# Performance work log

Hardware: AMD Instinct MI355X
Metric: run time of the kernel (lower is better)

## Reference

```python
import jax, jax.numpy as jnp
import numpy as np

EPS = 1e-5
NUM_GRAPHS = 64


def _linear(x, W, b):
    return x @ W + b


def setup_inputs() -> dict:
    key = jax.random.key(0)
    ks = jax.random.split(key, 32)
    N, E, IN, EF, H, ED, T, L, C = 25000, 400000, 128, 16, 32, 32, 4, 2, 1
    F = H            # F_in (divide_input=False)
    Fo = H // T      # F_out per tower

    def w(k, shape):
        return jax.random.normal(k, shape, jnp.float32) / np.sqrt(shape[-2])

    inp = {
        'x': jax.random.normal(ks[0], (N, IN), jnp.float32),
        'edge_attr': jax.random.normal(ks[1], (E, EF), jnp.float32),
        'edge_weight': jax.random.uniform(ks[2], (E,), jnp.float32),
        'edge_index': jax.random.randint(ks[3], (2, E), 0, N),
        'batch': jnp.sort(jax.random.randint(ks[4], (N,), 0, NUM_GRAPHS)),
        'node_W': w(ks[5], (IN, H)), 'node_b': jnp.zeros((H,), jnp.float32),
        'edge_W': w(ks[6], (EF, ED)), 'edge_b': jnp.zeros((ED,), jnp.float32),
        'enc_W': w(ks[7], (L, ED, F)), 'enc_b': jnp.zeros((L, F), jnp.float32),
        'pre_W': w(ks[8], (L, T, 3 * F, F)), 'pre_b': jnp.zeros((L, T, F), jnp.float32),
        'post_W': w(ks[9], (L, T, 13 * F, Fo)), 'post_b': jnp.zeros((L, T, Fo), jnp.float32),
        'lin_W': w(ks[10], (L, H, H)), 'lin_b': jnp.zeros((L, H), jnp.float32),
        'bn_g': jnp.ones((L, H), jnp.float32), 'bn_b': jnp.zeros((L, H), jnp.float32),
        'mlp_W1': w(ks[11], (H, H)), 'mlp_b1': jnp.zeros((H,), jnp.float32),
        'mlp_W2': w(ks[12], (H, H // 2)), 'mlp_b2': jnp.zeros((H // 2,), jnp.float32),
        'mlp_W3': w(ks[13], (H // 2, C)), 'mlp_b3': jnp.zeros((C,), jnp.float32),
    }
    return inp


def reference(x, edge_attr, edge_weight, node_W, node_b, edge_W, edge_b,
              enc_W, enc_b, pre_W, pre_b, post_W, post_b, lin_W, lin_b,
              bn_g, bn_b, mlp_W1, mlp_b1, mlp_W2, mlp_b2, mlp_W3, mlp_b3,
              edge_index, batch):
    N = x.shape[0]
    L, T = pre_W.shape[0], pre_W.shape[1]
    src, dst = edge_index[0], edge_index[1]

    # degree-based scalers (PNA): avg_deg_log = mean_n log(deg_n + 1)
    deg = jax.ops.segment_sum(jnp.ones((src.shape[0],), x.dtype), dst, num_segments=N)
    avg_deg_log = jnp.mean(jnp.log(deg + 1.0))
    degc = jnp.clip(deg, 1.0)[:, None, None]          # [N,1,1]
    log_deg = jnp.log(degc + 1.0)
    amp = log_deg / avg_deg_log                        # amplification scaler
    att = avg_deg_log / log_deg                        # attenuation scaler
    has_edge = (deg > 0)[:, None, None]

    h = _linear(x, node_W, node_b)                     # node_emb  [N,H]
    e = _linear(edge_attr, edge_W, edge_b)             # edge_emb  [E,ED]

    for l in range(L):
        el = _linear(e, enc_W[l], enc_b[l])            # edge_encoder [E,F]
        m_in = jnp.concatenate([h[dst], h[src], el], axis=-1)      # [E,3F]
        msg = jnp.einsum('ef,tfg->etg', m_in, pre_W[l]) + pre_b[l]  # per-tower pre_nn [E,T,F]
        msg = msg * edge_weight[:, None, None]
        s = jax.ops.segment_sum(msg, dst, num_segments=N)
        s2 = jax.ops.segment_sum(msg * msg, dst, num_segments=N)
        mean = s / degc
        std = jnp.sqrt(jax.nn.relu(s2 / degc - mean * mean) + EPS)
        mn = jnp.where(has_edge, jax.ops.segment_min(msg, dst, num_segments=N), 0.0)
        mx = jnp.where(has_edge, jax.ops.segment_max(msg, dst, num_segments=N), 0.0)
        agg = jnp.concatenate([mean, mn, mx, std], axis=-1)            # [N,T,4F]
        agg = jnp.concatenate([agg, agg * amp, agg * att], axis=-1)    # [N,T,12F]
        out = jnp.concatenate(
            [jnp.broadcast_to(h[:, None, :], (N, T, h.shape[-1])), agg], axis=-1)  # [N,T,13F]
        out = jnp.einsum('ntf,tfg->ntg', out, post_W[l]) + post_b[l]   # post_nn [N,T,Fo]
        out = out.reshape(N, -1) @ lin_W[l] + lin_b[l]                 # [N,H]
        mu = jnp.mean(out, axis=0)
        var = jnp.var(out, axis=0)
        out = (out - mu) / jnp.sqrt(var + EPS) * bn_g[l] + bn_b[l]     # BatchNorm (batch stats)
        h = jax.nn.relu(out)

    g = jax.ops.segment_sum(h, batch, num_segments=NUM_GRAPHS)        # global_add_pool
    g = jax.nn.relu(_linear(g, mlp_W1, mlp_b1))
    g = jax.nn.relu(_linear(g, mlp_W2, mlp_b2))
    return _linear(g, mlp_W3, mlp_b3)
```

## Files before the change

kernel.cpp:

```cpp
#include <hip/hip_runtime.h>

constexpr float kEps = 1e-5f;

typedef _Float16 h2 __attribute__((ext_vector_type(2)));
typedef float f2v __attribute__((ext_vector_type(2)));

__device__ __forceinline__ unsigned short f2bf(float x) {
  unsigned int u = __float_as_uint(x);
  unsigned int r = (u + 0x7fffu + ((u >> 16) & 1u)) >> 16;
  return (unsigned short)r;
}
__device__ __forceinline__ float bflo(unsigned int u) { return __uint_as_float(u << 16); }
__device__ __forceinline__ float bfhi(unsigned int u) { return __uint_as_float(u & 0xffff0000u); }
__device__ __forceinline__ unsigned int packbf(float a, float b) {
  return (unsigned int)f2bf(a) | ((unsigned int)f2bf(b) << 16);
}
__device__ __forceinline__ unsigned int pkh2(float a, float b) {
  h2 v; v.x = (_Float16)a; v.y = (_Float16)b;
  return __builtin_bit_cast(unsigned int, v);
}
__device__ __forceinline__ float dot2a(h2 a, h2 b, float c) {
#if __has_builtin(__builtin_amdgcn_fdot2)
  return __builtin_amdgcn_fdot2(a, b, c, false);
#else
  return c + (float)a.x * (float)b.x + (float)a.y * (float)b.y;
#endif
}
__device__ __forceinline__ h2 ash2(unsigned int u) { return __builtin_bit_cast(h2, u); }
__device__ __forceinline__ f2v fma2(f2v a, f2v b, f2v c) { return __builtin_elementwise_fma(a, b, c); }
__device__ __forceinline__ f2v unbf2(unsigned int u) { f2v r; r.x = bflo(u); r.y = bfhi(u); return r; }


__global__ void zero_kernel(int* __restrict__ a, int* __restrict__ b,
                            float* __restrict__ bnb, int n) {
  int i = blockIdx.x * blockDim.x + threadIdx.x;
  if (i < n) { a[i] = 0; b[i] = 0; }
  if (i < 128) bnb[i] = 0.f;
}

__global__ void hist_kernel(const int* __restrict__ dst, int* __restrict__ deg, int E) {
  int e = blockIdx.x * blockDim.x + threadIdx.x;
  if (e < E) atomicAdd(&deg[dst[e]], 1);
}

__global__ void scan1_kernel(const int* __restrict__ deg, int* __restrict__ off,
                             int* __restrict__ part, int N) {
  __shared__ int sm[1024];
  int i = blockIdx.x * 1024 + threadIdx.x;
  int v = (i < N) ? deg[i] : 0;
  sm[threadIdx.x] = v;
  __syncthreads();
  for (int o = 1; o < 1024; o <<= 1) {
    int t = (threadIdx.x >= o) ? sm[threadIdx.x - o] : 0;
    __syncthreads();
    sm[threadIdx.x] += t;
    __syncthreads();
  }
  if (i < N) off[i] = sm[threadIdx.x] - v;
  if (threadIdx.x == 1023) part[blockIdx.x] = sm[1023];
}

__global__ void scan2_kernel(int* __restrict__ part, int* __restrict__ off, int nb, int N) {
  if (threadIdx.x == 0) {
    int run = 0;
    for (int b = 0; b < nb; b++) { int p = part[b]; part[b] = run; run += p; }
    off[N] = run;
  }
}

__global__ void scan3_kernel(int* __restrict__ off, const int* __restrict__ part, int N) {
  int i = blockIdx.x * 1024 + threadIdx.x;
  if (i < N) off[i] += part[blockIdx.x];
}

__global__ void fill_kernel(const int* __restrict__ src, const int* __restrict__ dst,
                            const float* __restrict__ ew, const float4* __restrict__ eattr4,
                            const int* __restrict__ off, int* __restrict__ cnt,
                            int* __restrict__ srcs, float* __restrict__ ews,
                            uint4* __restrict__ eg16, int E) {
  int e = blockIdx.x * blockDim.x + threadIdx.x;
  if (e < E) {
    int d = dst[e];
    int slot = off[d] + atomicAdd(&cnt[d], 1);
    srcs[slot] = src[e];
    ews[slot] = ew[e];
    float4 a = eattr4[e * 4 + 0], b = eattr4[e * 4 + 1];
    float4 c = eattr4[e * 4 + 2], q = eattr4[e * 4 + 3];
    uint4 u0, u1;
    u0.x = pkh2(a.x, a.y); u0.y = pkh2(a.z, a.w);
    u0.z = pkh2(b.x, b.y); u0.w = pkh2(b.z, b.w);
    u1.x = pkh2(c.x, c.y); u1.y = pkh2(c.z, c.w);
    u1.z = pkh2(q.x, q.y); u1.w = pkh2(q.z, q.w);
    eg16[(size_t)slot * 2 + 0] = u0;
    eg16[(size_t)slot * 2 + 1] = u1;
  }
}

__global__ void adl_kernel(const int* __restrict__ deg, float* __restrict__ adl, int N) {
  __shared__ float sm[1024];
  float s = 0.f;
  for (int n = threadIdx.x; n < N; n += 1024) s += logf((float)deg[n] + 1.f);
  sm[threadIdx.x] = s;
  __syncthreads();
  for (int o = 512; o > 0; o >>= 1) {
    if (threadIdx.x < o) sm[threadIdx.x] += sm[threadIdx.x + o];
    __syncthreads();
  }
  if (threadIdx.x == 0) adl[0] = sm[0];
}

__global__ void node_emb_kernel(const float* __restrict__ x, const float* __restrict__ W,
                                const float* __restrict__ b, float* __restrict__ h, int N) {
  int n = blockIdx.x * 8 + (threadIdx.x >> 5);
  int j = threadIdx.x & 31;
  if (n >= N) return;
  float acc = b[j];
  const float4* x4 = (const float4*)(x + (size_t)n * 128);
#pragma unroll
  for (int q = 0; q < 32; q++) {
    float4 v = x4[q];
    acc += v.x * W[(4 * q + 0) * 32 + j];
    acc += v.y * W[(4 * q + 1) * 32 + j];
    acc += v.z * W[(4 * q + 2) * 32 + j];
    acc += v.w * W[(4 * q + 3) * 32 + j];
  }
  h[n * 32 + j] = acc;
}

__global__ void fuse_kernel(const float* __restrict__ edge_W, const float* __restrict__ edge_b,
                            const float* __restrict__ enc_W, const float* __restrict__ enc_b,
                            const float* __restrict__ pre_W, const float* __restrict__ pre_b,
                            float* __restrict__ Wf, float* __restrict__ bf) {
  __shared__ float tW[2][16][32];
  __shared__ float tb[2][32];
  int tid = threadIdx.x;
  for (int i = tid; i < 1024; i += 256) {
    int l = i >> 9, r = (i >> 5) & 15, c = i & 31;
    float s = 0.f;
    for (int k = 0; k < 32; k++) s += edge_W[r * 32 + k] * enc_W[(l * 32 + k) * 32 + c];
    tW[l][r][c] = s;
  }
  for (int i = tid; i < 64; i += 256) {
    int l = i >> 5, c = i & 31;
    float s = enc_b[l * 32 + c];
    for (int k = 0; k < 32; k++) s += edge_b[k] * enc_W[(l * 32 + k) * 32 + c];
    tb[l][c] = s;
  }
  __syncthreads();
  for (int i = tid; i < 4096; i += 256) {
    int l = i >> 11, t = (i >> 9) & 3, r = (i >> 5) & 15, c = i & 31;
    float s = 0.f;
    for (int k = 0; k < 32; k++) s += tW[l][r][k] * pre_W[((l * 4 + t) * 96 + 64 + k) * 32 + c];
    Wf[i] = s;
  }
  for (int i = tid; i < 256; i += 256) {
    int l = i >> 7, t = (i >> 5) & 3, c = i & 31;
    float s = pre_b[(l * 4 + t) * 32 + c];
    for (int k = 0; k < 32; k++) s += tb[l][k] * pre_W[((l * 4 + t) * 96 + 64 + k) * 32 + c];
    bf[i] = s;
  }
}

__global__ __launch_bounds__(256) void prep_kernel(
    const float* __restrict__ h, const float* __restrict__ preW,
    const float* __restrict__ bfv, unsigned short* __restrict__ qB,
    unsigned short* __restrict__ AB, int N) {
  __shared__ float hs[16][32];
  int tid = threadIdx.x;
  int c = tid & 127, half = tid >> 7;
  int t = c >> 5, g = c & 31;
  float ws[32], wd[32];
  {
    const float* pS = preW + (t * 96 + 32) * 32 + g;
    const float* pD = preW + (t * 96) * 32 + g;
#pragma unroll
    for (int k = 0; k < 32; k++) { ws[k] = pS[k * 32]; wd[k] = pD[k * 32]; }
  }
  float bc = bfv[c];
  int base = blockIdx.x * 16;
  for (int i = tid; i < 512; i += 256) {
    int nn = i >> 5;
    hs[nn][i & 31] = (base + nn < N) ? h[(size_t)(base + nn) * 32 + (i & 31)] : 0.f;
  }
  __syncthreads();
#pragma unroll
  for (int nn = 0; nn < 8; ++nn) {
    int nl = half + 2 * nn;
    int n = base + nl;
    if (n >= N) continue;
    float qa = 0.f, Aa = bc;
#pragma unroll
    for (int k = 0; k < 32; k++) {
      float hk = hs[nl][k];
      qa = fmaf(hk, ws[k], qa);
      Aa = fmaf(hk, wd[k], Aa);
    }
    qB[(size_t)n * 128 + c] = f2bf(qa);
    AB[(size_t)n * 128 + c] = f2bf(Aa);
  }
}

__global__ __launch_bounds__(256) void bnprep_kernel(
    const float* __restrict__ pre, const float* __restrict__ bnv,
    const float* __restrict__ gamma, const float* __restrict__ beta,
    const float* __restrict__ preW, const float* __restrict__ bfv,
    float* __restrict__ h, unsigned short* __restrict__ qB,
    unsigned short* __restrict__ AB, int N) {
  __shared__ float hs[16][32];
  int tid = threadIdx.x;
  int base = blockIdx.x * 16;
  float invN = 1.f / (float)N;
  for (int idx = tid; idx < 512; idx += 256) {
    int nn = idx >> 5, j = idx & 31;
    int n = base + nn;
    float v = 0.f;
    if (n < N) {
      float mu = bnv[j] * invN;
      float var = bnv[32 + j] * invN - mu * mu;
      float is = rsqrtf(var + kEps);
      v = fmaxf((pre[(size_t)n * 32 + j] - mu) * is * gamma[j] + beta[j], 0.f);
      h[(size_t)n * 32 + j] = v;
    }
    hs[nn][j] = v;
  }
  int c = tid & 127, half = tid >> 7;
  int t = c >> 5, g = c & 31;
  float ws[32], wd[32];
  {
    const float* pS = preW + (t * 96 + 32) * 32 + g;
    const float* pD = preW + (t * 96) * 32 + g;
#pragma unroll
    for (int k = 0; k < 32; k++) { ws[k] = pS[k * 32]; wd[k] = pD[k * 32]; }
  }
  float bc = bfv[c];
  __syncthreads();
#pragma unroll
  for (int nn = 0; nn < 8; ++nn) {
    int nl = half + 2 * nn;
    int n = base + nl;
    if (n >= N) continue;
    float qa = 0.f, Aa = bc;
#pragma unroll
    for (int k = 0; k < 32; k++) {
      float hk = hs[nl][k];
      qa = fmaf(hk, ws[k], qa);
      Aa = fmaf(hk, wd[k], Aa);
    }
    qB[(size_t)n * 128 + c] = f2bf(qa);
    AB[(size_t)n * 128 + c] = f2bf(Aa);
  }
}

#define DOTE(F0, F1, UA, UB)                                         \
  F0 = dot2a(ash2(UA.x), w0[0], F0); F1 = dot2a(ash2(UA.x), w1[0], F1); \
  F0 = dot2a(ash2(UA.y), w0[1], F0); F1 = dot2a(ash2(UA.y), w1[1], F1); \
  F0 = dot2a(ash2(UA.z), w0[2], F0); F1 = dot2a(ash2(UA.z), w1[2], F1); \
  F0 = dot2a(ash2(UA.w), w0[3], F0); F1 = dot2a(ash2(UA.w), w1[3], F1); \
  F0 = dot2a(ash2(UB.x), w0[4], F0); F1 = dot2a(ash2(UB.x), w1[4], F1); \
  F0 = dot2a(ash2(UB.y), w0[5], F0); F1 = dot2a(ash2(UB.y), w1[5], F1); \
  F0 = dot2a(ash2(UB.z), w0[6], F0); F1 = dot2a(ash2(UB.z), w1[6], F1); \
  F0 = dot2a(ash2(UB.w), w0[7], F0); F1 = dot2a(ash2(UB.w), w1[7], F1);

#define STATACC(V0, V1)                                                    \
  s0a += V0; sq0 = fmaf(V0, V0, sq0); mn0 = fminf(mn0, V0); mx0 = fmaxf(mx0, V0); \
  s1a += V1; sq1 = fmaf(V1, V1, sq1); mn1 = fminf(mn1, V1); mx1 = fmaxf(mx1, V1);

__global__ __launch_bounds__(256, 4) void agg10b_kernel(
    const unsigned int* __restrict__ qB, const unsigned int* __restrict__ AB,
    const int* __restrict__ coff, const int* __restrict__ srcs,
    const float* __restrict__ ews, const uint4* __restrict__ eg16,
    const float* __restrict__ Wf, unsigned int* __restrict__ stats, int N) {
  int lane = threadIdx.x & 63;
  int wv = (blockIdx.x * blockDim.x + threadIdx.x) >> 6;
  int nwaves = (gridDim.x * blockDim.x) >> 6;
  int t = lane >> 4, g0 = (2 * lane) & 31;
  h2 w0[8], w1[8];
  {
    const float* p = Wf + t * 512 + g0;
#pragma unroll
    for (int k = 0; k < 8; k++) {
      w0[k].x = (_Float16)p[(2 * k) * 32];     w0[k].y = (_Float16)p[(2 * k + 1) * 32];
      w1[k].x = (_Float16)p[(2 * k) * 32 + 1]; w1[k].y = (_Float16)p[(2 * k + 1) * 32 + 1];
    }
  }
  for (int n = wv; n < N; n += nwaves) {
    unsigned int au = AB[(size_t)n * 64 + lane];
    float a0 = bflo(au), a1 = bfhi(au);
    int beg = coff[n], end = coff[n + 1];
    int dg = end - beg;
    float s0a = 0.f, s1a = 0.f, sq0 = 0.f, sq1 = 0.f;
    float mn0 = 1e30f, mn1 = 1e30f, mx0 = -1e30f, mx1 = -1e30f;

    int i = beg;
    unsigned int q0 = 0, q1 = 0, q2 = 0, q3 = 0;
    int sc0 = 0, sc1 = 0, sc2 = 0, sc3 = 0;
    if (i + 4 <= end) {
      int t0 = srcs[i], t1 = srcs[i + 1], t2 = srcs[i + 2], t3 = srcs[i + 3];
      q0 = qB[(size_t)t0 * 64 + lane];
      q1 = qB[(size_t)t1 * 64 + lane];
      q2 = qB[(size_t)t2 * 64 + lane];
      q3 = qB[(size_t)t3 * 64 + lane];
    }
    if (i + 8 <= end) { sc0 = srcs[i + 4]; sc1 = srcs[i + 5]; sc2 = srcs[i + 6]; sc3 = srcs[i + 7]; }
    for (; i + 4 <= end; i += 4) {
      unsigned int nq0 = 0, nq1 = 0, nq2 = 0, nq3 = 0;
      if (i + 8 <= end) {
        nq0 = qB[(size_t)sc0 * 64 + lane];
        nq1 = qB[(size_t)sc1 * 64 + lane];
        nq2 = qB[(size_t)sc2 * 64 + lane];
        nq3 = qB[(size_t)sc3 * 64 + lane];
      }
      float w0s = ews[i], w1s = ews[i + 1], w2s = ews[i + 2], w3s = ews[i + 3];
      const uint4* ep = eg16 + (size_t)i * 2;
      uint4 eA0 = ep[0], eA1 = ep[1], eB0 = ep[2], eB1 = ep[3];
      uint4 eC0 = ep[4], eC1 = ep[5], eD0 = ep[6], eD1 = ep[7];
      if (i + 12 <= end) { sc0 = srcs[i + 8]; sc1 = srcs[i + 9]; sc2 = srcs[i + 10]; sc3 = srcs[i + 11]; }
      float f00 = 0.f, f10 = 0.f, f01 = 0.f, f11 = 0.f;
      float f02 = 0.f, f12 = 0.f, f03 = 0.f, f13 = 0.f;
      DOTE(f00, f10, eA0, eA1)
      DOTE(f01, f11, eB0, eB1)
      DOTE(f02, f12, eC0, eC1)
      DOTE(f03, f13, eD0, eD1)
      float v0, v1;
      v0 = (a0 + bflo(q0) + f00) * w0s; v1 = (a1 + bfhi(q0) + f10) * w0s; STATACC(v0, v1)
      v0 = (a0 + bflo(q1) + f01) * w1s; v1 = (a1 + bfhi(q1) + f11) * w1s; STATACC(v0, v1)
      v0 = (a0 + bflo(q2) + f02) * w2s; v1 = (a1 + bfhi(q2) + f12) * w2s; STATACC(v0, v1)
      v0 = (a0 + bflo(q3) + f03) * w3s; v1 = (a1 + bfhi(q3) + f13) * w3s; STATACC(v0, v1)
      q0 = nq0; q1 = nq1; q2 = nq2; q3 = nq3;
    }
    for (; i < end; ++i) {
      int s = srcs[i];
      unsigned int q = qB[(size_t)s * 64 + lane];
      float w = ews[i];
      const uint4* ep = eg16 + (size_t)i * 2;
      uint4 ea = ep[0], eb = ep[1];
      float f0 = 0.f, f1 = 0.f;
      DOTE(f0, f1, ea, eb)
      float v0 = (a0 + bflo(q) + f0) * w;
      float v1 = (a1 + bfhi(q) + f1) * w;
      STATACC(v0, v1)
    }
    if (dg == 0) { mn0 = 0.f; mx0 = 0.f; mn1 = 0.f; mx1 = 0.f; }
    float inv = 1.f / (float)(dg > 0 ? dg : 1);
    float mean0 = s0a * inv, mean1 = s1a * inv;
    float sd0 = sqrtf(fmaxf(sq0 * inv - mean0 * mean0, 0.f) + kEps);
    float sd1 = sqrtf(fmaxf(sq1 * inv - mean1 * mean1, 0.f) + kEps);
    unsigned int* sp = stats + (size_t)n * 256;
    sp[0 * 64 + lane] = packbf(mean0, mean1);
    sp[1 * 64 + lane] = packbf(mn0, mn1);
    sp[2 * 64 + lane] = packbf(mx0, mx1);
    sp[3 * 64 + lane] = packbf(sd0, sd1);
  }
}

__global__ __launch_bounds__(256) void post_kernel(
    const float* __restrict__ h, const unsigned int* __restrict__ stats,
    const int* __restrict__ coff, const float* __restrict__ adl,
    const float* __restrict__ postW, const float* __restrict__ postB,
    const float* __restrict__ linW, const float* __restrict__ linB,
    float* __restrict__ pre, float* __restrict__ bn, int N) {
  __shared__ unsigned int pwp[208 * 32];
  __shared__ unsigned int stu[4][256];
  __shared__ float red[8][32];
  int tid = threadIdx.x;
  for (int i = tid; i < 6656; i += 256) {
    int r = i >> 5, cc = i & 31, tP = cc >> 3, gq = cc & 7;
    float lo = postW[tP * 3328 + (2 * r) * 8 + gq];
    float hi = postW[tP * 3328 + (2 * r + 1) * 8 + gq];
    pwp[i] = packbf(lo, hi);
  }
  __syncthreads();

  int wave = tid >> 6, lane = tid & 63;
  int c = lane & 31, hh = lane >> 5;
  int tP = c >> 3;
  float adN = adl[0];
  float bs = 0.f, bq = 0.f;

  for (int n = blockIdx.x * 4 + wave; n < N; n += gridDim.x * 4) {
    {
      uint4 su = ((const uint4*)stats)[(size_t)n * 64 + lane];
      ((uint4*)stu[wave])[lane] = su;
    }
    int dg = coff[n + 1] - coff[n];
    float degc = (float)(dg > 0 ? dg : 1);
    float ad = adN / (float)N;
    float ld = logf(degc + 1.f);
    float amp = ld / ad, att = ad / ld;

    float acc = (hh == 0) ? postB[tP * 8 + (c & 7)] : 0.f;
    const float4* h4 = (const float4*)(h + (size_t)n * 32);
#pragma unroll
    for (int q4 = 0; q4 < 4; q4++) {
      float4 hv = h4[hh * 4 + q4];
      int r0 = hh * 8 + q4 * 2;
      unsigned int u0 = pwp[r0 * 32 + c], u1 = pwp[(r0 + 1) * 32 + c];
      acc = fmaf(hv.x, bflo(u0), acc);
      acc = fmaf(hv.y, bfhi(u0), acc);
      acc = fmaf(hv.z, bflo(u1), acc);
      acc = fmaf(hv.w, bfhi(u1), acc);
    }
    f2v ym, ya, yt;
    ym.x = 0.f; ym.y = 0.f; ya = ym; yt = ym;
#pragma unroll 8
    for (int jj = 0; jj < 32; jj++) {
      int sIdx = hh * 2 + (jj >> 4);
      unsigned int sv = stu[wave][sIdx * 64 + tP * 16 + (jj & 15)];
      f2v v2 = unbf2(sv);
      int rm = 16 + hh * 32 + jj;
      f2v um = unbf2(pwp[rm * 32 + c]);
      f2v ua = unbf2(pwp[(rm + 64) * 32 + c]);
      f2v ut = unbf2(pwp[(rm + 128) * 32 + c]);
      ym = fma2(v2, um, ym);
      ya = fma2(v2, ua, ya);
      yt = fma2(v2, ut, yt);
    }
    acc += ym.x + ym.y;
    acc = fmaf(amp, ya.x + ya.y, acc);
    acc = fmaf(att, yt.x + yt.y, acc);
    acc += __shfl_xor(acc, 32);
    float o = linB[c];
#pragma unroll
    for (int k = 0; k < 32; k++) {
      float a = __shfl(acc, k);
      o = fmaf(a, linW[k * 32 + c], o);
    }
    if (lane < 32) {
      pre[(size_t)n * 32 + c] = o;
      bs += o;
      bq = fmaf(o, o, bq);
    }
  }

  __syncthreads();
  if (lane < 32) {
    red[wave * 2 + 0][c] = bs;
    red[wave * 2 + 1][c] = bq;
  }
  __syncthreads();
  if (tid < 64) {
    int which = tid >> 5, cc = tid & 31;
    float s = red[0 * 2 + which][cc] + red[1 * 2 + which][cc] +
              red[2 * 2 + which][cc] + red[3 * 2 + which][cc];
    atomicAdd(&bn[which * 32 + cc], s);
  }
}


__device__ __forceinline__ int lower_bound_dev(const int* a, int n, int key) {
  int lo = 0, hi = n;
  while (lo < hi) {
    int m = (lo + hi) >> 1;
    if (a[m] < key) lo = m + 1; else hi = m;
  }
  return lo;
}

__global__ void pool2_kernel(const float* __restrict__ pre, const float* __restrict__ bnv,
                             const float* __restrict__ gamma, const float* __restrict__ beta,
                             const int* __restrict__ batch, float* __restrict__ gp, int N) {
  int gi = blockIdx.x;
  int lo = lower_bound_dev(batch, N, gi);
  int hi = lower_bound_dev(batch, N, gi + 1);
  __shared__ float part[8][32];
  int j = threadIdx.x & 31, ch = threadIdx.x >> 5;
  float invN = 1.f / (float)N;
  float mu = bnv[j] * invN;
  float var = bnv[32 + j] * invN - mu * mu;
  float is = rsqrtf(var + kEps);
  float gm = gamma[j], bt = beta[j];
  float s = 0.f;
  for (int n = lo + ch; n < hi; n += 8)
    s += fmaxf((pre[(size_t)n * 32 + j] - mu) * is * gm + bt, 0.f);
  part[ch][j] = s;
  __syncthreads();
  if (threadIdx.x < 32) {
    float t = 0.f;
    for (int c2 = 0; c2 < 8; c2++) t += part[c2][j];
    gp[gi * 32 + j] = t;
  }
}

__global__ void mlp_kernel(const float* __restrict__ gp,
                           const float* __restrict__ W1, const float* __restrict__ b1,
                           const float* __restrict__ W2, const float* __restrict__ b2,
                           const float* __restrict__ W3, const float* __restrict__ b3,
                           float* __restrict__ out) {
  __shared__ float g1[64 * 32];
  __shared__ float g2[64 * 16];
  int tid = threadIdx.x;
  for (int i = tid; i < 2048; i += 256) {
    int r = i >> 5, c = i & 31;
    float s = b1[c];
    for (int k = 0; k < 32; k++) s += gp[r * 32 + k] * W1[k * 32 + c];
    g1[i] = fmaxf(s, 0.f);
  }
  __syncthreads();
  for (int i = tid; i < 1024; i += 256) {
    int r = i >> 4, c = i & 15;
    float s = b2[c];
    for (int k = 0; k < 32; k++) s += g1[r * 32 + k] * W2[k * 16 + c];
    g2[i] = fmaxf(s, 0.f);
  }
  __syncthreads();
  if (tid < 64) {
    float s = b3[0];
    for (int k = 0; k < 16; k++) s += g2[tid * 16 + k] * W3[k];
    out[tid] = s;
  }
}


extern "C" void kernel_launch(void* const* d_in, const int* in_sizes, int n_in,
                              void* d_out, int out_size, void* d_ws, size_t ws_size,
                              hipStream_t stream) {
  (void)n_in; (void)out_size; (void)ws_size;
  const float* x     = (const float*)d_in[0];
  const float* eattr = (const float*)d_in[1];
  const float* ew    = (const float*)d_in[2];
  const int*   eidx  = (const int*)d_in[3];
  const int*   batch = (const int*)d_in[4];
  const float* nodeW = (const float*)d_in[5];
  const float* nodeB = (const float*)d_in[6];
  const float* edgeW = (const float*)d_in[7];
  const float* edgeB = (const float*)d_in[8];
  const float* encW  = (const float*)d_in[9];
  const float* encB  = (const float*)d_in[10];
  const float* preW  = (const float*)d_in[11];
  const float* preB  = (const float*)d_in[12];
  const float* postW = (const float*)d_in[13];
  const float* postB = (const float*)d_in[14];
  const float* linW  = (const float*)d_in[15];
  const float* linB  = (const float*)d_in[16];
  const float* bnG   = (const float*)d_in[17];
  const float* bnB   = (const float*)d_in[18];
  const float* W1    = (const float*)d_in[19];
  const float* b1    = (const float*)d_in[20];
  const float* W2    = (const float*)d_in[21];
  const float* b2    = (const float*)d_in[22];
  const float* W3    = (const float*)d_in[23];
  const float* b3    = (const float*)d_in[24];
  float* out = (float*)d_out;

  int N = in_sizes[0] / 128;
  int E = in_sizes[2];
  const int* srcp = eidx;
  const int* dstp = eidx + E;

  char* wsb = (char*)d_ws;
  size_t woff = 0;
  auto alloc = [&](size_t bytes) -> void* {
    void* p = (void*)(wsb + woff);
    woff += (bytes + 255) & ~(size_t)255;
    return p;
  };
  int* deg   = (int*)alloc((size_t)N * 4);
  int* cnt   = (int*)alloc((size_t)N * 4);
  int* coff  = (int*)alloc((size_t)(N + 1) * 4);
  int* part  = (int*)alloc(64 * 4);
  int* srcs  = (int*)alloc((size_t)E * 4);
  float* ews = (float*)alloc((size_t)E * 4);
  unsigned int* eg16 = (unsigned int*)alloc((size_t)E * 32);
  float* h    = (float*)alloc((size_t)N * 32 * 4);
  float* pre  = (float*)alloc((size_t)N * 32 * 4);
  float* adl  = (float*)alloc(256);
  float* bnbuf = (float*)alloc(2 * 64 * 4);
  float* gp   = (float*)alloc(64 * 32 * 4);
  float* WfB  = (float*)alloc(2 * 4 * 16 * 32 * 4);
  float* bfB  = (float*)alloc(2 * 4 * 32 * 4);
  unsigned short* qB  = (unsigned short*)alloc((size_t)N * 128 * 2);
  unsigned short* AB  = (unsigned short*)alloc((size_t)N * 128 * 2);
  unsigned int* stats = (unsigned int*)alloc((size_t)N * 256 * 4);

  int nb = (N + 1023) / 1024;
  zero_kernel<<<(N + 255) / 256, 256, 0, stream>>>(deg, cnt, bnbuf, N);
  hist_kernel<<<(E + 255) / 256, 256, 0, stream>>>(dstp, deg, E);
  scan1_kernel<<<nb, 1024, 0, stream>>>(deg, coff, part, N);
  scan2_kernel<<<1, 64, 0, stream>>>(part, coff, nb, N);
  scan3_kernel<<<nb, 1024, 0, stream>>>(coff, part, N);
  fill_kernel<<<(E + 255) / 256, 256, 0, stream>>>(srcp, dstp, ew, (const float4*)eattr,
                                                   coff, cnt, srcs, ews, (uint4*)eg16, E);
  adl_kernel<<<1, 1024, 0, stream>>>(deg, adl, N);
  node_emb_kernel<<<(N + 7) / 8, 256, 0, stream>>>(x, nodeW, nodeB, h, N);
  fuse_kernel<<<1, 256, 0, stream>>>(edgeW, edgeB, encW, encB, preW, preB, WfB, bfB);

  prep_kernel<<<(N + 15) / 16, 256, 0, stream>>>(h, preW, bfB, qB, AB, N);
  agg10b_kernel<<<2048, 256, 0, stream>>>(
      (const unsigned int*)qB, (const unsigned int*)AB, coff, srcs, ews,
      (const uint4*)eg16, WfB, stats, N);
  post_kernel<<<640, 256, 0, stream>>>(
      h, stats, coff, adl, postW, postB, linW, linB, pre, bnbuf, N);
  bnprep_kernel<<<(N + 15) / 16, 256, 0, stream>>>(
      pre, bnbuf, bnG, bnB, preW + 12288, bfB + 128, h, qB, AB, N);
  agg10b_kernel<<<2048, 256, 0, stream>>>(
      (const unsigned int*)qB, (const unsigned int*)AB, coff, srcs, ews,
      (const uint4*)eg16, WfB + 2048, stats, N);
  post_kernel<<<640, 256, 0, stream>>>(
      h, stats, coff, adl, postW + 13312, postB + 32, linW + 1024, linB + 32,
      pre, bnbuf + 64, N);
  pool2_kernel<<<64, 256, 0, stream>>>(pre, bnbuf + 64, bnG + 32, bnB + 32, batch, gp, N);
  mlp_kernel<<<1, 256, 0, stream>>>(gp, W1, b1, W2, b2, W3, b3, out);
}
```

Baseline: 375.4 us.

## Fold post_nn into lin weights and compute post stage with bf16 MFMA

Precomputes a combined post_W×lin_W matrix per layer, split into identity, amplification and attenuation sections and laid out as bf16 MFMA B-fragments, plus a fused bias. The per-node post stage becomes a 16-node-tile GEMM using 16x16x32 bf16 MFMA over the aggregated statistics and a new bf16 copy of h, with the degree scalers applied after accumulation. This replaces the scalar per-node FMA loop and the shuffle-based lin matvec. The cost is an extra bf16 h buffer written in the prep kernels, a small weight-fusion kernel, and bf16 rounding of the fused weights.

```diff
diff --git a/kernel.cpp b/kernel.cpp
--- a/kernel.cpp
+++ b/kernel.cpp
@@ -4,6 +4,8 @@
 
 typedef _Float16 h2 __attribute__((ext_vector_type(2)));
 typedef float f2v __attribute__((ext_vector_type(2)));
+typedef short bf16x8 __attribute__((ext_vector_type(8)));
+typedef float f32x4v __attribute__((ext_vector_type(4)));
 
 __device__ __forceinline__ unsigned short f2bf(float x) {
   unsigned int u = __float_as_uint(x);
@@ -27,8 +29,10 @@
 #endif
 }
 __device__ __forceinline__ h2 ash2(unsigned int u) { return __builtin_bit_cast(h2, u); }
-__device__ __forceinline__ f2v fma2(f2v a, f2v b, f2v c) { return __builtin_elementwise_fma(a, b, c); }
-__device__ __forceinline__ f2v unbf2(unsigned int u) { f2v r; r.x = bflo(u); r.y = bfhi(u); return r; }
+__device__ __forceinline__ f32x4v mfma16(uint4 a, uint4 b, f32x4v c) {
+  return __builtin_amdgcn_mfma_f32_16x16x32_bf16(
+      __builtin_bit_cast(bf16x8, a), __builtin_bit_cast(bf16x8, b), c, 0, 0, 0);
+}
 
 
 __global__ void zero_kernel(int* __restrict__ a, int* __restrict__ b,
@@ -161,10 +165,51 @@
   }
 }
 
+__global__ void fuse2_kernel(const float* __restrict__ postW_, const float* __restrict__ postB_,
+                             const float* __restrict__ linW_, const float* __restrict__ linB_,
+                             unsigned int* __restrict__ Bfrag, float* __restrict__ bias2) {
+  int l = blockIdx.x;
+  const float* postW = postW_ + (size_t)l * 13312;
+  const float* postB = postB_ + l * 32;
+  const float* linW = linW_ + l * 1024;
+  const float* linB = linB_ + l * 32;
+  unsigned int* Bf = Bfrag + (size_t)l * 26112;
+  int tid = threadIdx.x;
+  for (int idx = tid; idx < 26112; idx += 256) {
+    int d = idx & 3, lane = (idx >> 2) & 63;
+    int ks = (idx >> 8) % 17, jt = (idx >> 8) / 17;
+    int jcol = (jt & 1) * 16 + (lane & 15);
+    int jsec = jt >> 1;
+    float v[2];
+#pragma unroll
+    for (int e2 = 0; e2 < 2; ++e2) {
+      int k = ks * 32 + ((lane >> 4) << 3) + 2 * d + e2;
+      float s = 0.f;
+      if (k < 512) {
+        int st = k >> 7, t = (k >> 5) & 3, g = k & 31;
+        int rowW = 32 + jsec * 128 + st * 32 + g;
+        for (int q = 0; q < 8; ++q)
+          s += postW[t * 3328 + rowW * 8 + q] * linW[(t * 8 + q) * 32 + jcol];
+      } else if (jsec == 0) {
+        int kk = k - 512;
+        for (int c = 0; c < 32; ++c)
+          s += postW[(c >> 3) * 3328 + kk * 8 + (c & 7)] * linW[c * 32 + jcol];
+      }
+      v[e2] = s;
+    }
+    Bf[idx] = packbf(v[0], v[1]);
+  }
+  if (tid < 32) {
+    float s = linB[tid];
+    for (int c = 0; c < 32; ++c) s += postB[c] * linW[c * 32 + tid];
+    bias2[l * 32 + tid] = s;
+  }
+}
+
 __global__ __launch_bounds__(256) void prep_kernel(
     const float* __restrict__ h, const float* __restrict__ preW,
     const float* __restrict__ bfv, unsigned short* __restrict__ qB,
-    unsigned short* __restrict__ AB, int N) {
+    unsigned short* __restrict__ AB, unsigned int* __restrict__ hB, int N) {
   __shared__ float hs[16][32];
   int tid = threadIdx.x;
   int c = tid & 127, half = tid >> 7;
@@ -183,6 +228,11 @@
     hs[nn][i & 31] = (base + nn < N) ? h[(size_t)(base + nn) * 32 + (i & 31)] : 0.f;
   }
   __syncthreads();
+  {
+    int nn = tid >> 4, w = tid & 15;
+    int n = base + nn;
+    if (n < N) hB[(size_t)n * 16 + w] = packbf(hs[nn][2 * w], hs[nn][2 * w + 1]);
+  }
 #pragma unroll
   for (int nn = 0; nn < 8; ++nn) {
     int nl = half + 2 * nn;
@@ -205,7 +255,7 @@
     const float* __restrict__ gamma, const float* __restrict__ beta,
     const float* __restrict__ preW, const float* __restrict__ bfv,
     float* __restrict__ h, unsigned short* __restrict__ qB,
-    unsigned short* __restrict__ AB, int N) {
+    unsigned short* __restrict__ AB, unsigned int* __restrict__ hB, int N) {
   __shared__ float hs[16][32];
   int tid = threadIdx.x;
   int base = blockIdx.x * 16;
@@ -234,6 +284,11 @@
   }
   float bc = bfv[c];
   __syncthreads();
+  {
+    int nn = tid >> 4, w = tid & 15;
+    int n = base + nn;
+    if (n < N) hB[(size_t)n * 16 + w] = packbf(hs[nn][2 * w], hs[nn][2 * w + 1]);
+  }
 #pragma unroll
   for (int nn = 0; nn < 8; ++nn) {
     int nl = half + 2 * nn;
@@ -353,96 +408,75 @@
   }
 }
 
-__global__ __launch_bounds__(256) void post_kernel(
-    const float* __restrict__ h, const unsigned int* __restrict__ stats,
+__global__ __launch_bounds__(256) void postm_kernel(
+    const uint4* __restrict__ statsU4, const uint4* __restrict__ hBU4,
     const int* __restrict__ coff, const float* __restrict__ adl,
-    const float* __restrict__ postW, const float* __restrict__ postB,
-    const float* __restrict__ linW, const float* __restrict__ linB,
-    float* __restrict__ pre, float* __restrict__ bn, int N) {
-  __shared__ unsigned int pwp[208 * 32];
-  __shared__ unsigned int stu[4][256];
-  __shared__ float red[8][32];
-  int tid = threadIdx.x;
-  for (int i = tid; i < 6656; i += 256) {
-    int r = i >> 5, cc = i & 31, tP = cc >> 3, gq = cc & 7;
-    float lo = postW[tP * 3328 + (2 * r) * 8 + gq];
-    float hi = postW[tP * 3328 + (2 * r + 1) * 8 + gq];
-    pwp[i] = packbf(lo, hi);
-  }
-  __syncthreads();
-
-  int wave = tid >> 6, lane = tid & 63;
-  int c = lane & 31, hh = lane >> 5;
-  int tP = c >> 3;
-  float adN = adl[0];
-  float bs = 0.f, bq = 0.f;
-
-  for (int n = blockIdx.x * 4 + wave; n < N; n += gridDim.x * 4) {
-    {
-      uint4 su = ((const uint4*)stats)[(size_t)n * 64 + lane];
-      ((uint4*)stu[wave])[lane] = su;
-    }
-    int dg = coff[n + 1] - coff[n];
-    float degc = (float)(dg > 0 ? dg : 1);
-    float ad = adN / (float)N;
-    float ld = logf(degc + 1.f);
-    float amp = ld / ad, att = ad / ld;
-
-    float acc = (hh == 0) ? postB[tP * 8 + (c & 7)] : 0.f;
-    const float4* h4 = (const float4*)(h + (size_t)n * 32);
-#pragma unroll
-    for (int q4 = 0; q4 < 4; q4++) {
-      float4 hv = h4[hh * 4 + q4];
-      int r0 = hh * 8 + q4 * 2;
-      unsigned int u0 = pwp[r0 * 32 + c], u1 = pwp[(r0 + 1) * 32 + c];
-      acc = fmaf(hv.x, bflo(u0), acc);
-      acc = fmaf(hv.y, bfhi(u0), acc);
-      acc = fmaf(hv.z, bflo(u1), acc);
-      acc = fmaf(hv.w, bfhi(u1), acc);
-    }
-    f2v ym, ya, yt;
-    ym.x = 0.f; ym.y = 0.f; ya = ym; yt = ym;
-#pragma unroll 8
-    for (int jj = 0; jj < 32; jj++) {
-      int sIdx = hh * 2 + (jj >> 4);
-      unsigned int sv = stu[wave][sIdx * 64 + tP * 16 + (jj & 15)];
-      f2v v2 = unbf2(sv);
-      int rm = 16 + hh * 32 + jj;
-      f2v um = unbf2(pwp[rm * 32 + c]);
-      f2v ua = unbf2(pwp[(rm + 64) * 32 + c]);
-      f2v ut = unbf2(pwp[(rm + 128) * 32 + c]);
-      ym = fma2(v2, um, ym);
-      ya = fma2(v2, ua, ya);
-      yt = fma2(v2, ut, yt);
-    }
-    acc += ym.x + ym.y;
-    acc = fmaf(amp, ya.x + ya.y, acc);
-    acc = fmaf(att, yt.x + yt.y, acc);
-    acc += __shfl_xor(acc, 32);
-    float o = linB[c];
-#pragma unroll
-    for (int k = 0; k < 32; k++) {
-      float a = __shfl(acc, k);
-      o = fmaf(a, linW[k * 32 + c], o);
-    }
-    if (lane < 32) {
-      pre[(size_t)n * 32 + c] = o;
-      bs += o;
-      bq = fmaf(o, o, bq);
-    }
-  }
-
-  __syncthreads();
-  if (lane < 32) {
-    red[wave * 2 + 0][c] = bs;
-    red[wave * 2 + 1][c] = bq;
-  }
-  __syncthreads();
-  if (tid < 64) {
-    int which = tid >> 5, cc = tid & 31;
-    float s = red[0 * 2 + which][cc] + red[1 * 2 + which][cc] +
-              red[2 * 2 + which][cc] + red[3 * 2 + which][cc];
-    atomicAdd(&bn[which * 32 + cc], s);
+    const unsigned int* __restrict__ BfragL, const float* __restrict__ bias2,
+    float* __restrict__ pre, float* __restrict__ bn, int N, int ntcnt) {
+  __shared__ uint4 Bs[6 * 6 * 64];
+  int tid = threadIdx.x, wave = tid >> 6, lane = tid & 63;
+  int nt = blockIdx.x * 4 + wave;
+  int ntb = nt * 16;
+  int ntbC = (nt < ntcnt ? nt : ntcnt - 1) * 16;
+  const uint4* Bf4 = (const uint4*)BfragL;
+
+  f32x4v acc[6];
+#pragma unroll
+  for (int jt = 0; jt < 6; ++jt) { acc[jt].x = 0.f; acc[jt].y = 0.f; acc[jt].z = 0.f; acc[jt].w = 0.f; }
+
+  int ksBase = 0;
+  for (int stage = 0; stage < 3; ++stage) {
+    int ksN = (stage == 2) ? 5 : 6;
+    for (int i = tid; i < 6 * ksN * 64; i += 256) {
+      int ln = i & 63, rest = i >> 6;
+      int ksl = rest % ksN, jt = rest / ksN;
+      Bs[(jt * 6 + ksl) * 64 + ln] = Bf4[(jt * 17 + ksBase + ksl) * 64 + ln];
+    }
+    __syncthreads();
+    for (int ksl = 0; ksl < ksN; ++ksl) {
+      int ks = ksBase + ksl;
+      uint4 a;
+      if (ks < 16) {
+        a = statsU4[(size_t)(ntbC + (lane & 15)) * 64 + (ks >> 2) * 16 + (ks & 3) * 4 + (lane >> 4)];
+      } else {
+        a = hBU4[(size_t)(ntbC + (lane & 15)) * 4 + (lane >> 4)];
+      }
+#pragma unroll
+      for (int jt = 0; jt < 6; ++jt)
+        acc[jt] = mfma16(a, Bs[(jt * 6 + ksl) * 64 + lane], acc[jt]);
+    }
+    __syncthreads();
+    ksBase += ksN;
+  }
+
+  float adv = adl[0] / (float)N;
+  int j0 = lane & 15;
+  float bs0 = 0.f, bq0 = 0.f, bs1 = 0.f, bq1 = 0.f;
+#pragma unroll
+  for (int reg = 0; reg < 4; ++reg) {
+    int n = ntb + ((lane >> 4) << 2) + reg;
+    if (n < N) {
+      int dg = coff[n + 1] - coff[n];
+      float degc = (float)(dg > 0 ? dg : 1);
+      float ld = logf(degc + 1.f);
+      float amp = ld / adv, att = adv / ld;
+      float v0 = bias2[j0]      + acc[0][reg] + amp * acc[2][reg] + att * acc[4][reg];
+      float v1 = bias2[16 + j0] + acc[1][reg] + amp * acc[3][reg] + att * acc[5][reg];
+      pre[(size_t)n * 32 + j0] = v0;
+      pre[(size_t)n * 32 + 16 + j0] = v1;
+      bs0 += v0; bq0 = fmaf(v0, v0, bq0);
+      bs1 += v1; bq1 = fmaf(v1, v1, bq1);
+    }
+  }
+  bs0 += __shfl_xor(bs0, 16); bs0 += __shfl_xor(bs0, 32);
+  bq0 += __shfl_xor(bq0, 16); bq0 += __shfl_xor(bq0, 32);
+  bs1 += __shfl_xor(bs1, 16); bs1 += __shfl_xor(bs1, 32);
+  bq1 += __shfl_xor(bq1, 16); bq1 += __shfl_xor(bq1, 32);
+  if (lane < 16) {
+    atomicAdd(&bn[j0], bs0);
+    atomicAdd(&bn[32 + j0], bq0);
+    atomicAdd(&bn[16 + j0], bs1);
+    atomicAdd(&bn[48 + j0], bq1);
   }
 }
 
@@ -570,9 +604,15 @@
   float* bfB  = (float*)alloc(2 * 4 * 32 * 4);
   unsigned short* qB  = (unsigned short*)alloc((size_t)N * 128 * 2);
   unsigned short* AB  = (unsigned short*)alloc((size_t)N * 128 * 2);
-  unsigned int* stats = (unsigned int*)alloc((size_t)N * 256 * 4);
+  unsigned int* stats = (unsigned int*)alloc((size_t)(N + 16) * 256 * 4);
+  unsigned int* hB    = (unsigned int*)alloc((size_t)(N + 16) * 16 * 4);
+  unsigned int* Bfrag = (unsigned int*)alloc(2 * 26112 * 4);
+  float* bias2 = (float*)alloc(2 * 32 * 4);
 
   int nb = (N + 1023) / 1024;
+  int ntcnt = (N + 15) / 16;
+  int grid_pm = (ntcnt + 3) / 4;
+
   zero_kernel<<<(N + 255) / 256, 256, 0, stream>>>(deg, cnt, bnbuf, N);
   hist_kernel<<<(E + 255) / 256, 256, 0, stream>>>(dstp, deg, E);
   scan1_kernel<<<nb, 1024, 0, stream>>>(deg, coff, part, N);
@@ -583,21 +623,23 @@
   adl_kernel<<<1, 1024, 0, stream>>>(deg, adl, N);
   node_emb_kernel<<<(N + 7) / 8, 256, 0, stream>>>(x, nodeW, nodeB, h, N);
   fuse_kernel<<<1, 256, 0, stream>>>(edgeW, edgeB, encW, encB, preW, preB, WfB, bfB);
-
-  prep_kernel<<<(N + 15) / 16, 256, 0, stream>>>(h, preW, bfB, qB, AB, N);
+  fuse2_kernel<<<2, 256, 0, stream>>>(postW, postB, linW, linB, Bfrag, bias2);
+
+  prep_kernel<<<(N + 15) / 16, 256, 0, stream>>>(h, preW, bfB, qB, AB, hB, N);
   agg10b_kernel<<<2048, 256, 0, stream>>>(
       (const unsigned int*)qB, (const unsigned int*)AB, coff, srcs, ews,
       (const uint4*)eg16, WfB, stats, N);
-  post_kernel<<<640, 256, 0, stream>>>(
-      h, stats, coff, adl, postW, postB, linW, linB, pre, bnbuf, N);
+  postm_kernel<<<grid_pm, 256, 0, stream>>>(
+      (const uint4*)stats, (const uint4*)hB, coff, adl, Bfrag, bias2,
+      pre, bnbuf, N, ntcnt);
   bnprep_kernel<<<(N + 15) / 16, 256, 0, stream>>>(
-      pre, bnbuf, bnG, bnB, preW + 12288, bfB + 128, h, qB, AB, N);
+      pre, bnbuf, bnG, bnB, preW + 12288, bfB + 128, h, qB, AB, hB, N);
   agg10b_kernel<<<2048, 256, 0, stream>>>(
       (const unsigned int*)qB, (const unsigned int*)AB, coff, srcs, ews,
       (const uint4*)eg16, WfB + 2048, stats, N);
-  post_kernel<<<640, 256, 0, stream>>>(
-      h, stats, coff, adl, postW + 13312, postB + 32, linW + 1024, linB + 32,
-      pre, bnbuf + 64, N);
+  postm_kernel<<<grid_pm, 256, 0, stream>>>(
+      (const uint4*)stats, (const uint4*)hB, coff, adl, Bfrag + 26112, bias2 + 32,
+      pre, bnbuf + 64, N, ntcnt);
   pool2_kernel<<<64, 256, 0, stream>>>(pre, bnbuf + 64, bnG + 32, bnB + 32, batch, gp, N);
   mlp_kernel<<<1, 256, 0, stream>>>(gp, W1, b1, W2, b2, W3, b3, out);
 }
```

Result: slower. 487.8 us (+29.9%).
